# Optimization experiments

Measured on AMD Instinct MI355X. Metric: run time of the kernel, lower is better.

## Reference

```python
import jax, jax.numpy as jnp
import numpy as np

N = 50000        # num nodes
E = 800000       # num edges (avg degree 16)
IN_DIM = 64
OUT_DIM = 64
PE_DIM = 24
HEADS = 2
HID = OUT_DIM * HEADS  # 128


def setup_inputs() -> dict:
    key = jax.random.key(0)
    ks = jax.random.split(key, 16)
    std = 0.1  # trunc_normal_(std=0.1) init in the torch module
    return {
        "x": jax.random.normal(ks[0], (N, IN_DIM), jnp.float32),
        "pe_index": jax.random.randint(ks[1], (2, E), 0, N, jnp.int32),
        "pe_val": jax.random.normal(ks[2], (E, PE_DIM), jnp.float32),
        # edge-weight MLP (blocks): input proj, one residual FFN block, final proj
        "W_in": jax.random.normal(ks[3], (PE_DIM, HID), jnp.float32) * std,
        "b_in": jnp.zeros((HID,), jnp.float32),
        "W1": jax.random.normal(ks[4], (HID, HID), jnp.float32) * std,
        "b1": jnp.zeros((HID,), jnp.float32),
        "W2": jax.random.normal(ks[5], (HID, HID), jnp.float32) * std,
        "b2": jnp.zeros((HID,), jnp.float32),
        "W_fin": jax.random.normal(ks[6], (HID, HID), jnp.float32) * std,
        "b_fin": jnp.zeros((HID,), jnp.float32),
        # node feature -> multi-head projection
        "W_x": jax.random.normal(ks[7], (IN_DIM, HID), jnp.float32) * std,
        "b_x": jnp.zeros((HID,), jnp.float32),
        # per-head output bias
        "head_bias": jnp.zeros((1, HEADS, OUT_DIM), jnp.float32),
        # final out projection
        "W_out": jax.random.normal(ks[8], (HID, OUT_DIM), jnp.float32) * std,
        "b_out": jnp.zeros((OUT_DIM,), jnp.float32),
    }


def _edge_mlp(pe, W_in, b_in, W1, b1, W2, b2, W_fin, b_fin):
    # Linear(pe_dim->hid), then residual block [GELU, Linear, GELU, Linear, +res], then Linear(hid->hid)
    g = lambda t: jax.nn.gelu(t, approximate=False)  # torch nn.GELU default = exact erf
    x0 = pe @ W_in + b_in                     # [E, HID]
    h = g(x0) @ W1 + b1
    h = g(h) @ W2 + b2
    x0 = h + x0                               # ResidualLayer: x + x_res
    return x0 @ W_fin + b_fin                 # [E, HID]


def reference(x, pe_index, pe_val, W_in, b_in, W1, b1, W2, b2, W_fin, b_fin,
              W_x, b_x, head_bias, W_out, b_out):
    tgt = pe_index[0]  # messages aggregate to edge_index[0]
    src = pe_index[1]
    score = _edge_mlp(pe_val, W_in, b_in, W1, b1, W2, b2, W_fin, b_fin)
    score = score.reshape(-1, HEADS, OUT_DIM)                 # [E, H, D]
    xh = (x @ W_x + b_x).reshape(-1, HEADS, OUT_DIM)          # [N, H, D]
    msg = xh[src] * score                                     # gather-multiply
    wV = jax.ops.segment_sum(msg, tgt, num_segments=N)        # scatter-add [N, H, D]
    deg = jax.ops.segment_sum(jnp.ones((msg.shape[0],), jnp.float32), tgt, num_segments=N)
    wV = wV / jnp.maximum(deg, 1.0)[:, None, None]            # average=True -> mean aggregation
    h = (wV + head_bias).reshape(-1, HEADS * OUT_DIM)
    return h @ W_out + b_out                                  # out_proj: [N, OUT_DIM]
```

## Files before the change

### kernel.cpp

```cpp
#include <hip/hip_runtime.h>
#include <hip/hip_bf16.h>
#include <math.h>

#define NN 50000
#define EE 800000
#define HID 128
#define PED 24
#define IND 64
#define OUTD 64
#define EBLK 128
#define AKS 136

typedef short bf16x8 __attribute__((ext_vector_type(8)));
typedef float f32x4 __attribute__((ext_vector_type(4)));

__device__ __forceinline__ float gelu_fast(float x) {
    float x2 = x * x;
    float t = __builtin_fmaf(x2, -0.07135481627f, -1.5957691216f);
    float e = __expf(x * t);
    return x * __builtin_amdgcn_rcpf(1.0f + e);
}
__device__ __forceinline__ unsigned short f2bf(float f) {
    unsigned int u = __float_as_uint(f);
    u = (u + 0x7fffu + ((u >> 16) & 1u)) >> 16;
    return (unsigned short)u;
}
__device__ __forceinline__ unsigned int pkbf2(float a, float b) {
    __hip_bfloat162 h = __float22bfloat162_rn(make_float2(a, b));
    return *reinterpret_cast<unsigned int*>(&h);
}
__device__ __forceinline__ float bflo(unsigned int u) {
    return __uint_as_float(u << 16);
}
__device__ __forceinline__ float bfhi(unsigned int u) {
    return __uint_as_float(u & 0xffff0000u);
}

__global__ __launch_bounds__(256) void pre_kernel(
    const float* __restrict__ x, const float* __restrict__ W_x,
    const float* __restrict__ b_x, unsigned short* __restrict__ xhb,
    const float* __restrict__ W_in, const float* __restrict__ W1,
    const float* __restrict__ W2, const float* __restrict__ Wf,
    unsigned short* __restrict__ WT_in, unsigned short* __restrict__ WT1,
    unsigned short* __restrict__ WT2, unsigned short* __restrict__ WTf,
    float* __restrict__ wV, int* __restrict__ cnt) {
    int bx = blockIdx.x;
    if (bx < 6250) {
        int gid = bx * 256 + threadIdx.x;
        int n = gid >> 5;
        int q = gid & 31;
        *(float4*)&wV[(size_t)n * HID + q * 4] = make_float4(0.f, 0.f, 0.f, 0.f);
        const float* xr = x + (size_t)n * IND;
        float4 acc = *(const float4*)&b_x[q * 4];
#pragma unroll 8
        for (int k = 0; k < IND; k++) {
            float xk = xr[k];
            float4 w = *(const float4*)&W_x[k * HID + q * 4];
            acc.x += xk * w.x; acc.y += xk * w.y;
            acc.z += xk * w.z; acc.w += xk * w.w;
        }
        uint2 p;
        p.x = pkbf2(acc.x, acc.y);
        p.y = pkbf2(acc.z, acc.w);
        ((uint2*)&xhb[(size_t)n * HID])[q] = p;
    } else {
        int idx = (bx - 6250) * 256 + threadIdx.x;
        if (idx < NN) cnt[idx] = 0;
        if (idx < 4096) {
            int j = idx >> 5, k = idx & 31;
            WT_in[idx] = f2bf(k < PED ? W_in[k * HID + j] : 0.f);
        } else if (idx < 4096 + 16384) {
            int i = idx - 4096; int j = i >> 7, k = i & 127;
            WT1[i] = f2bf(W1[k * HID + j]);
        } else if (idx < 4096 + 32768) {
            int i = idx - 4096 - 16384; int j = i >> 7, k = i & 127;
            WT2[i] = f2bf(W2[k * HID + j]);
        } else if (idx < 4096 + 49152) {
            int i = idx - 4096 - 32768; int j = i >> 7, k = i & 127;
            WTf[i] = f2bf(Wf[k * HID + j]);
        }
    }
}

__global__ __launch_bounds__(256) void hist_kernel(const int* __restrict__ pe_idx,
                                                   int* __restrict__ cnt) {
    int e4 = blockIdx.x * 256 + threadIdx.x;
    if (e4 < EE / 4) {
        int4 t = *(const int4*)&pe_idx[e4 * 4];
        atomicAdd(&cnt[t.x], 1);
        atomicAdd(&cnt[t.y], 1);
        atomicAdd(&cnt[t.z], 1);
        atomicAdd(&cnt[t.w], 1);
    }
}

__global__ __launch_bounds__(1024) void scan_kernel(const int* __restrict__ cnt,
                                                    int* __restrict__ woff) {
    __shared__ int s_w[16];
    int tid = threadIdx.x;
    const int chunk = 52;
    int base = tid * chunk;
    int end = base + chunk; if (end > NN) end = NN;
    int s = 0;
    if (base + chunk <= NN) {
#pragma unroll
        for (int i = 0; i < 13; i++) {
            int4 v4 = *(const int4*)&cnt[base + i * 4];
            s += v4.x + v4.y + v4.z + v4.w;
        }
    } else {
        for (int i = base; i < end; i++) s += cnt[i];
    }
    int v = s;
    int lane = tid & 63, wid = tid >> 6;
#pragma unroll
    for (int d = 1; d < 64; d <<= 1) {
        int u = __shfl_up(v, d, 64);
        if (lane >= d) v += u;
    }
    if (lane == 63) s_w[wid] = v;
    __syncthreads();
    if (tid < 16) {
        int wv = s_w[tid];
#pragma unroll
        for (int d = 1; d < 16; d <<= 1) {
            int u = __shfl_up(wv, d, 64);
            if (tid >= d) wv += u;
        }
        s_w[tid] = wv;
    }
    __syncthreads();
    int exc = v - s + (wid ? s_w[wid - 1] : 0);
    int run = exc;
    for (int i = base; i < end; i++) { woff[i] = run; run += cnt[i]; }
}

__global__ __launch_bounds__(256) void scatter_kernel(const int* __restrict__ pe_idx,
                                                      int* __restrict__ woff,
                                                      int* __restrict__ perm) {
    int e4 = blockIdx.x * 256 + threadIdx.x;
    if (e4 < EE / 4) {
        int4 t = *(const int4*)&pe_idx[e4 * 4];
        int e = e4 * 4;
        perm[atomicAdd(&woff[t.x], 1)] = e + 0;
        perm[atomicAdd(&woff[t.y], 1)] = e + 1;
        perm[atomicAdd(&woff[t.z], 1)] = e + 2;
        perm[atomicAdd(&woff[t.w], 1)] = e + 3;
    }
}

__global__ __launch_bounds__(512, 4) void edge_kernel(
    const float* __restrict__ pe_val, const int* __restrict__ pe_idx,
    const int* __restrict__ perm, const unsigned short* __restrict__ xhb,
    const unsigned short* __restrict__ WT_in, const unsigned short* __restrict__ WT1,
    const unsigned short* __restrict__ WT2, const unsigned short* __restrict__ WTf,
    const float* __restrict__ b_in, const float* __restrict__ b1,
    const float* __restrict__ b2, const float* __restrict__ bfin,
    float* __restrict__ wV) {
    __shared__ __align__(16) unsigned short s_act[EBLK][AKS];
    __shared__ __align__(16) unsigned short s_W[HID][AKS];
    __shared__ int s_tgt[EBLK], s_src[EBLK];
    float* s_msg = (float*)&s_W[0][0];

    const int tid = threadIdx.x;
    const int lane = tid & 63;
    const int w = tid >> 6;
    const int cg = w & 3;
    const int eh = w >> 2;
    const int ebase = eh * 64;
    const int l15 = lane & 15;
    const int quad = lane >> 4;
    const long b0 = (long)blockIdx.x * EBLK;

    if (tid < EBLK) {
        int eid = perm[b0 + tid];
        s_tgt[tid] = pe_idx[eid];
        s_src[tid] = pe_idx[EE + eid];
    }
#pragma unroll
    for (int i = 0; i < 4; i++) {
        int idx = tid + i * 512; int r = idx >> 4, seg = idx & 15;
        *(uint4*)&s_W[r][seg * 8] = *(const uint4*)&WT1[r * HID + seg * 8];
    }
#pragma unroll
    for (int i = 0; i < 4; i++) {
        int idx = tid + i * 512; int e = idx >> 4, k2 = idx & 15;
        float2 v = make_float2(0.f, 0.f);
        if (k2 < 12) {
            int eid = perm[b0 + e];
            v = *(const float2*)&pe_val[(size_t)eid * PED + k2 * 2];
        }
        *(unsigned int*)&s_act[e][k2 * 2] = pkbf2(v.x, v.y);
    }
    __syncthreads();

    f32x4 C[2][4];
    uint2 x0pk[2][4];

    {
        float4 ba = *(const float4*)&b_in[(2 * cg + 0) * 16 + quad * 4];
        float4 bb = *(const float4*)&b_in[(2 * cg + 1) * 16 + quad * 4];
        f32x4 ci0 = {ba.x, ba.y, ba.z, ba.w};
        f32x4 ci1 = {bb.x, bb.y, bb.z, bb.w};
        bf16x8 a0 = *(const bf16x8*)&WT_in[((2 * cg + 0) * 16 + l15) * 32 + quad * 8];
        bf16x8 a1 = *(const bf16x8*)&WT_in[((2 * cg + 1) * 16 + l15) * 32 + quad * 8];
        __builtin_amdgcn_s_setprio(1);
#pragma unroll
        for (int u = 0; u < 4; u++) {
            bf16x8 bfr = *(const bf16x8*)&s_act[ebase + u * 16 + l15][quad * 8];
            C[0][u] = __builtin_amdgcn_mfma_f32_16x16x32_bf16(a0, bfr, ci0, 0, 0, 0);
            C[1][u] = __builtin_amdgcn_mfma_f32_16x16x32_bf16(a1, bfr, ci1, 0, 0, 0);
        }
        __builtin_amdgcn_s_setprio(0);
    }
    __syncthreads();
#pragma unroll
    for (int t = 0; t < 2; t++) {
        int ch0 = (2 * cg + t) * 16 + quad * 4;
#pragma unroll
        for (int u = 0; u < 4; u++) {
            int e = ebase + u * 16 + l15;
            f32x4 c = C[t][u];
            x0pk[t][u].x = pkbf2(c[0], c[1]);
            x0pk[t][u].y = pkbf2(c[2], c[3]);
            uint2 p;
            p.x = pkbf2(gelu_fast(c[0]), gelu_fast(c[1]));
            p.y = pkbf2(gelu_fast(c[2]), gelu_fast(c[3]));
            *(uint2*)&s_act[e][ch0] = p;
        }
    }
    __syncthreads();

#define GEMM128(BIAS)                                                          \
    {                                                                          \
        float4 ba_ = *(const float4*)&(BIAS)[(2 * cg + 0) * 16 + quad * 4];    \
        float4 bb_ = *(const float4*)&(BIAS)[(2 * cg + 1) * 16 + quad * 4];    \
        f32x4 ci0 = {ba_.x, ba_.y, ba_.z, ba_.w};                              \
        f32x4 ci1 = {bb_.x, bb_.y, bb_.z, bb_.w};                              \
        _Pragma("unroll") for (int u = 0; u < 4; u++) {                        \
            C[0][u] = ci0; C[1][u] = ci1;                                      \
        }                                                                      \
        __builtin_amdgcn_s_setprio(1);                                         \
        _Pragma("unroll") for (int ks = 0; ks < 4; ks++) {                     \
            bf16x8 a0 = *(const bf16x8*)&s_W[(2 * cg + 0) * 16 + l15]          \
                                            [ks * 32 + quad * 8];              \
            bf16x8 a1 = *(const bf16x8*)&s_W[(2 * cg + 1) * 16 + l15]          \
                                            [ks * 32 + quad * 8];              \
            _Pragma("unroll") for (int u = 0; u < 4; u++) {                    \
                bf16x8 bfr = *(const bf16x8*)&s_act[ebase + u * 16 + l15]      \
                                                   [ks * 32 + quad * 8];       \
                C[0][u] = __builtin_amdgcn_mfma_f32_16x16x32_bf16(a0, bfr,     \
                                                                  C[0][u], 0, 0, 0); \
                C[1][u] = __builtin_amdgcn_mfma_f32_16x16x32_bf16(a1, bfr,     \
                                                                  C[1][u], 0, 0, 0); \
            }                                                                  \
        }                                                                      \
        __builtin_amdgcn_s_setprio(0);                                         \
    }

#define PREFETCH_W(WT, DST)                                                    \
    _Pragma("unroll") for (int i = 0; i < 4; i++) {                            \
        int idx = tid + i * 512;                                               \
        DST[i] = *(const uint4*)&(WT)[(idx >> 4) * HID + (idx & 15) * 8];      \
    }
#define WRITE_W(SRC)                                                           \
    _Pragma("unroll") for (int i = 0; i < 4; i++) {                            \
        int idx = tid + i * 512; int r = idx >> 4, seg = idx & 15;             \
        *(uint4*)&s_W[r][seg * 8] = SRC[i];                                    \
    }

    uint4 wpre[4];
    PREFETCH_W(WT2, wpre);
    GEMM128(b1);
    __syncthreads();
#pragma unroll
    for (int t = 0; t < 2; t++) {
        int ch0 = (2 * cg + t) * 16 + quad * 4;
#pragma unroll
        for (int u = 0; u < 4; u++) {
            int e = ebase + u * 16 + l15;
            f32x4 c = C[t][u];
            uint2 p;
            p.x = pkbf2(gelu_fast(c[0]), gelu_fast(c[1]));
            p.y = pkbf2(gelu_fast(c[2]), gelu_fast(c[3]));
            *(uint2*)&s_act[e][ch0] = p;
        }
    }
    WRITE_W(wpre);
    __syncthreads();

    PREFETCH_W(WTf, wpre);
    GEMM128(b2);
    __syncthreads();
#pragma unroll
    for (int t = 0; t < 2; t++) {
        int ch0 = (2 * cg + t) * 16 + quad * 4;
#pragma unroll
        for (int u = 0; u < 4; u++) {
            int e = ebase + u * 16 + l15;
            f32x4 c = C[t][u];
            uint2 p;
            p.x = pkbf2(c[0] + bflo(x0pk[t][u].x), c[1] + bfhi(x0pk[t][u].x));
            p.y = pkbf2(c[2] + bflo(x0pk[t][u].y), c[3] + bfhi(x0pk[t][u].y));
            *(uint2*)&s_act[e][ch0] = p;
        }
    }
    WRITE_W(wpre);
    __syncthreads();

    GEMM128(bfin);
    uint2 xva[4];
#pragma unroll
    for (int i = 0; i < 4; i++) {
        int idx = tid + i * 512; int e = idx >> 5, c4 = idx & 31;
        xva[i] = ((const uint2*)&xhb[(size_t)s_src[e] * HID])[c4];
    }
    __syncthreads();
#pragma unroll
    for (int t = 0; t < 2; t++) {
        int ch0 = (2 * cg + t) * 16 + quad * 4;
#pragma unroll
        for (int u = 0; u < 4; u++) {
            int e = ebase + u * 16 + l15;
            f32x4 c = C[t][u];
            uint2 p;
            p.x = pkbf2(c[0], c[1]);
            p.y = pkbf2(c[2], c[3]);
            *(uint2*)&s_act[e][ch0] = p;
        }
    }
    __syncthreads();

#pragma unroll
    for (int i = 0; i < 4; i++) {
        int idx = tid + i * 512;
        int e = idx >> 5, c4 = idx & 31;
        uint2 xv = xva[i];
        uint2 sv = *(const uint2*)&s_act[e][c4 * 4];
        float4 m;
        m.x = bflo(xv.x) * bflo(sv.x);
        m.y = bfhi(xv.x) * bfhi(sv.x);
        m.z = bflo(xv.y) * bflo(sv.y);
        m.w = bfhi(xv.y) * bfhi(sv.y);
        *(float4*)&s_msg[e * HID + c4 * 4] = m;
    }
    uint2 xvb[4];
#pragma unroll
    for (int i = 0; i < 4; i++) {
        int idx = tid + (4 + i) * 512; int e = idx >> 5, c4 = idx & 31;
        xvb[i] = ((const uint2*)&xhb[(size_t)s_src[e] * HID])[c4];
    }
    __syncthreads();

    if (tid < 256) {
        const int h = tid >> 7;
        const int c = tid & 127;
        const int e0 = h * 32;
        float acc = 0.f;
        int prev = s_tgt[e0];
        bool firstseg = true;
        for (int e = e0; e < e0 + 32; e++) {
            int tg = s_tgt[e];
            if (tg != prev) {
                if (firstseg) atomicAdd(&wV[(size_t)prev * HID + c], acc);
                else          wV[(size_t)prev * HID + c] = acc;
                firstseg = false;
                acc = 0.f;
                prev = tg;
            }
            acc += s_msg[e * HID + c];
        }
        atomicAdd(&wV[(size_t)prev * HID + c], acc);
    }
    __syncthreads();

#pragma unroll
    for (int i = 0; i < 4; i++) {
        int idx = tid + (4 + i) * 512;
        int e = idx >> 5, c4 = idx & 31;
        uint2 xv = xvb[i];
        uint2 sv = *(const uint2*)&s_act[e][c4 * 4];
        float4 m;
        m.x = bflo(xv.x) * bflo(sv.x);
        m.y = bfhi(xv.x) * bfhi(sv.x);
        m.z = bflo(xv.y) * bflo(sv.y);
        m.w = bfhi(xv.y) * bfhi(sv.y);
        *(float4*)&s_msg[(e - 64) * HID + c4 * 4] = m;
    }
    __syncthreads();

    if (tid < 256) {
        const int h = tid >> 7;
        const int c = tid & 127;
        const int e0 = 64 + h * 32;
        float acc = 0.f;
        int prev = s_tgt[e0];
        bool firstseg = true;
        for (int e = e0; e < e0 + 32; e++) {
            int tg = s_tgt[e];
            if (tg != prev) {
                if (firstseg) atomicAdd(&wV[(size_t)prev * HID + c], acc);
                else          wV[(size_t)prev * HID + c] = acc;
                firstseg = false;
                acc = 0.f;
                prev = tg;
            }
            acc += s_msg[(e - 64) * HID + c];
        }
        atomicAdd(&wV[(size_t)prev * HID + c], acc);
    }
#undef GEMM128
#undef PREFETCH_W
#undef WRITE_W
}

__global__ __launch_bounds__(256) void out_kernel(
    const float* __restrict__ wV, const int* __restrict__ cnt,
    const float* __restrict__ head_bias, const float* __restrict__ W_out,
    const float* __restrict__ b_out, float* __restrict__ out) {
    int gid = blockIdx.x * 256 + threadIdx.x;
    int n = gid >> 4;
    int q = gid & 15;
    if (n >= NN) return;
    float inv = 1.0f / fmaxf((float)cnt[n], 1.0f);
    const float* wr = wV + (size_t)n * HID;
    float4 acc = *(const float4*)&b_out[q * 4];
#pragma unroll 4
    for (int k = 0; k < HID; k++) {
        float hv = wr[k] * inv + head_bias[k];
        float4 wv4 = *(const float4*)&W_out[k * OUTD + q * 4];
        acc.x += hv * wv4.x; acc.y += hv * wv4.y;
        acc.z += hv * wv4.z; acc.w += hv * wv4.w;
    }
    *(float4*)&out[(size_t)n * OUTD + q * 4] = acc;
}

extern "C" void kernel_launch(void* const* d_in, const int* in_sizes, int n_in,
                              void* d_out, int out_size, void* d_ws, size_t ws_size,
                              hipStream_t stream) {
    const float* x      = (const float*)d_in[0];
    const int*   pe_idx = (const int*)d_in[1];
    const float* pe_val = (const float*)d_in[2];
    const float* W_in   = (const float*)d_in[3];
    const float* b_in   = (const float*)d_in[4];
    const float* W1     = (const float*)d_in[5];
    const float* b1     = (const float*)d_in[6];
    const float* W2     = (const float*)d_in[7];
    const float* b2     = (const float*)d_in[8];
    const float* Wf     = (const float*)d_in[9];
    const float* bfin   = (const float*)d_in[10];
    const float* W_x    = (const float*)d_in[11];
    const float* b_x    = (const float*)d_in[12];
    const float* hb     = (const float*)d_in[13];
    const float* W_out  = (const float*)d_in[14];
    const float* b_out  = (const float*)d_in[15];
    float* out = (float*)d_out;

    float* wV   = (float*)d_ws;
    int*   cnt  = (int*)(wV + (size_t)NN * HID);
    int*   woff = cnt + NN;
    int*   perm = woff + NN;
    unsigned short* WT_in = (unsigned short*)(perm + EE);
    unsigned short* WT1   = WT_in + 128 * 32;
    unsigned short* WT2   = WT1 + 128 * 128;
    unsigned short* WTf   = WT2 + 128 * 128;
    unsigned short* xhb   = WTf + 128 * 128;

    pre_kernel<<<6250 + 208, 256, 0, stream>>>(x, W_x, b_x, xhb,
                                               W_in, W1, W2, Wf,
                                               WT_in, WT1, WT2, WTf, wV, cnt);
    hist_kernel<<<(EE / 4 + 255) / 256, 256, 0, stream>>>(pe_idx, cnt);
    scan_kernel<<<1, 1024, 0, stream>>>(cnt, woff);
    scatter_kernel<<<(EE / 4 + 255) / 256, 256, 0, stream>>>(pe_idx, woff, perm);

    edge_kernel<<<EE / EBLK, 512, 0, stream>>>(pe_val, pe_idx, perm, xhb,
                                               WT_in, WT1, WT2, WTf,
                                               b_in, b1, b2, bfin, wV);

    out_kernel<<<(NN * 16 + 255) / 256, 256, 0, stream>>>(wV, cnt, hb, W_out,
                                                          b_out, out);
}
```

Before: 693.5 us.

## Register-tile node GEMMs with shared weights and drop edge weight prefetch

The node projection in pre_kernel and the output projection in out_kernel now stage the weight matrix in shared memory. Each thread computes four nodes, so every weight load is reused across several rows instead of being re-read from global memory per node. In the edge kernel, the register prefetch of the next layer's weights is replaced by a direct global-to-shared copy after the epilogue. That lowers register pressure but exposes the load latency between the GEMM stages.

```diff
diff --git a/kernel.cpp b/kernel.cpp
--- a/kernel.cpp
+++ b/kernel.cpp
@@ -10,6 +10,8 @@
 #define OUTD 64
 #define EBLK 128
 #define AKS 136
+#define XNB 32
+#define ONB 64
 
 typedef short bf16x8 __attribute__((ext_vector_type(8)));
 typedef float f32x4 __attribute__((ext_vector_type(4)));
@@ -36,6 +38,7 @@
     return __uint_as_float(u & 0xffff0000u);
 }
 
+#define XHB ((NN + XNB - 1) / XNB)
 __global__ __launch_bounds__(256) void pre_kernel(
     const float* __restrict__ x, const float* __restrict__ W_x,
     const float* __restrict__ b_x, unsigned short* __restrict__ xhb,
@@ -45,26 +48,64 @@
     unsigned short* __restrict__ WT2, unsigned short* __restrict__ WTf,
     float* __restrict__ wV, int* __restrict__ cnt) {
     int bx = blockIdx.x;
-    if (bx < 6250) {
-        int gid = bx * 256 + threadIdx.x;
-        int n = gid >> 5;
-        int q = gid & 31;
-        *(float4*)&wV[(size_t)n * HID + q * 4] = make_float4(0.f, 0.f, 0.f, 0.f);
-        const float* xr = x + (size_t)n * IND;
-        float4 acc = *(const float4*)&b_x[q * 4];
-#pragma unroll 8
-        for (int k = 0; k < IND; k++) {
-            float xk = xr[k];
-            float4 w = *(const float4*)&W_x[k * HID + q * 4];
-            acc.x += xk * w.x; acc.y += xk * w.y;
-            acc.z += xk * w.z; acc.w += xk * w.w;
-        }
-        uint2 p;
-        p.x = pkbf2(acc.x, acc.y);
-        p.y = pkbf2(acc.z, acc.w);
-        ((uint2*)&xhb[(size_t)n * HID])[q] = p;
+    int tid = threadIdx.x;
+    if (bx < XHB) {
+        __shared__ float s_Wx[IND * HID];
+#pragma unroll
+        for (int i = 0; i < 8; i++) {
+            int idx = tid + i * 256;
+            *(float4*)&s_Wx[idx * 4] = *(const float4*)&W_x[idx * 4];
+        }
+#pragma unroll
+        for (int i = 0; i < 4; i++) {
+            int idx = tid + i * 256;
+            int n = bx * XNB + (idx >> 5);
+            if (n < NN)
+                *(float4*)&wV[(size_t)n * HID + (idx & 31) * 4] =
+                    make_float4(0.f, 0.f, 0.f, 0.f);
+        }
+        __syncthreads();
+        const int g = tid >> 5;
+        const int q = tid & 31;
+        const int nb = bx * XNB + g * 4;
+        float4 bb = *(const float4*)&b_x[q * 4];
+        f32x4 acc[4];
+        int nc[4];
+#pragma unroll
+        for (int j = 0; j < 4; j++) {
+            acc[j] = (f32x4){bb.x, bb.y, bb.z, bb.w};
+            int n = nb + j;
+            nc[j] = n < NN ? n : NN - 1;
+        }
+#pragma unroll
+        for (int k4 = 0; k4 < 16; k4++) {
+            float4 xv[4];
+#pragma unroll
+            for (int j = 0; j < 4; j++)
+                xv[j] = *(const float4*)&x[(size_t)nc[j] * IND + k4 * 4];
+#pragma unroll
+            for (int kk = 0; kk < 4; kk++) {
+                float4 w4 = *(const float4*)&s_Wx[(k4 * 4 + kk) * HID + q * 4];
+#pragma unroll
+                for (int j = 0; j < 4; j++) {
+                    float xs = ((const float*)&xv[j])[kk];
+                    acc[j][0] += xs * w4.x; acc[j][1] += xs * w4.y;
+                    acc[j][2] += xs * w4.z; acc[j][3] += xs * w4.w;
+                }
+            }
+        }
+#pragma unroll
+        for (int j = 0; j < 4; j++) {
+            int n = nb + j;
+            if (n < NN) {
+                uint2 p;
+                p.x = pkbf2(acc[j][0], acc[j][1]);
+                p.y = pkbf2(acc[j][2], acc[j][3]);
+                *(uint2*)&xhb[(size_t)n * HID + q * 4] = p;
+            }
+        }
     } else {
-        int idx = (bx - 6250) * 256 + threadIdx.x;
+        int idx = (bx - XHB) * 256 + tid;
         if (idx < NN) cnt[idx] = 0;
         if (idx < 4096) {
             int j = idx >> 5, k = idx & 31;
@@ -258,19 +299,12 @@
         __builtin_amdgcn_s_setprio(0);                                         \
     }
 
-#define PREFETCH_W(WT, DST)                                                    \
-    _Pragma("unroll") for (int i = 0; i < 4; i++) {                            \
-        int idx = tid + i * 512;                                               \
-        DST[i] = *(const uint4*)&(WT)[(idx >> 4) * HID + (idx & 15) * 8];      \
-    }
-#define WRITE_W(SRC)                                                           \
+#define STAGE_W(WT)                                                            \
     _Pragma("unroll") for (int i = 0; i < 4; i++) {                            \
         int idx = tid + i * 512; int r = idx >> 4, seg = idx & 15;             \
-        *(uint4*)&s_W[r][seg * 8] = SRC[i];                                    \
-    }
-
-    uint4 wpre[4];
-    PREFETCH_W(WT2, wpre);
+        *(uint4*)&s_W[r][seg * 8] = *(const uint4*)&(WT)[r * HID + seg * 8];   \
+    }
+
     GEMM128(b1);
     __syncthreads();
 #pragma unroll
@@ -286,10 +320,9 @@
             *(uint2*)&s_act[e][ch0] = p;
         }
     }
-    WRITE_W(wpre);
-    __syncthreads();
-
-    PREFETCH_W(WTf, wpre);
+    STAGE_W(WT2);
+    __syncthreads();
+
     GEMM128(b2);
     __syncthreads();
 #pragma unroll
@@ -305,7 +338,7 @@
             *(uint2*)&s_act[e][ch0] = p;
         }
     }
-    WRITE_W(wpre);
+    STAGE_W(WTf);
     __syncthreads();
 
     GEMM128(bfin);
@@ -410,29 +443,65 @@
         atomicAdd(&wV[(size_t)prev * HID + c], acc);
     }
 #undef GEMM128
-#undef PREFETCH_W
-#undef WRITE_W
+#undef STAGE_W
 }
 
 __global__ __launch_bounds__(256) void out_kernel(
     const float* __restrict__ wV, const int* __restrict__ cnt,
     const float* __restrict__ head_bias, const float* __restrict__ W_out,
     const float* __restrict__ b_out, float* __restrict__ out) {
-    int gid = blockIdx.x * 256 + threadIdx.x;
-    int n = gid >> 4;
-    int q = gid & 15;
-    if (n >= NN) return;
-    float inv = 1.0f / fmaxf((float)cnt[n], 1.0f);
-    const float* wr = wV + (size_t)n * HID;
-    float4 acc = *(const float4*)&b_out[q * 4];
-#pragma unroll 4
-    for (int k = 0; k < HID; k++) {
-        float hv = wr[k] * inv + head_bias[k];
-        float4 wv4 = *(const float4*)&W_out[k * OUTD + q * 4];
-        acc.x += hv * wv4.x; acc.y += hv * wv4.y;
-        acc.z += hv * wv4.z; acc.w += hv * wv4.w;
-    }
-    *(float4*)&out[(size_t)n * OUTD + q * 4] = acc;
+    __shared__ float s_Wo[HID * OUTD];
+    __shared__ float s_hb[HID];
+    int tid = threadIdx.x;
+#pragma unroll
+    for (int i = 0; i < 8; i++) {
+        int idx = tid + i * 256;
+        *(float4*)&s_Wo[idx * 4] = *(const float4*)&W_out[idx * 4];
+    }
+    if (tid < 32) *(float4*)&s_hb[tid * 4] = *(const float4*)&head_bias[tid * 4];
+    __syncthreads();
+
+    const int g = tid >> 4;
+    const int q = tid & 15;
+    const int nb = blockIdx.x * ONB + g * 4;
+    float4 bb = *(const float4*)&b_out[q * 4];
+    f32x4 acc[4];
+    float inv[4];
+    int nc[4];
+#pragma unroll
+    for (int j = 0; j < 4; j++) {
+        acc[j] = (f32x4){bb.x, bb.y, bb.z, bb.w};
+        int n = nb + j;
+        nc[j] = n < NN ? n : NN - 1;
+        inv[j] = 1.0f / fmaxf((float)cnt[nc[j]], 1.0f);
+    }
+#pragma unroll
+    for (int k4 = 0; k4 < 32; k4++) {
+        float4 wrv[4];
+#pragma unroll
+        for (int j = 0; j < 4; j++)
+            wrv[j] = *(const float4*)&wV[(size_t)nc[j] * HID + k4 * 4];
+#pragma unroll
+        for (int kk = 0; kk < 4; kk++) {
+            int k = k4 * 4 + kk;
+            float4 w4 = *(const float4*)&s_Wo[k * OUTD + q * 4];
+            float hbk = s_hb[k];
+#pragma unroll
+            for (int j = 0; j < 4; j++) {
+                float hv = __builtin_fmaf(((const float*)&wrv[j])[kk], inv[j], hbk);
+                acc[j][0] += hv * w4.x; acc[j][1] += hv * w4.y;
+                acc[j][2] += hv * w4.z; acc[j][3] += hv * w4.w;
+            }
+        }
+    }
+#pragma unroll
+    for (int j = 0; j < 4; j++) {
+        int n = nb + j;
+        if (n < NN) {
+            float4 o = {acc[j][0], acc[j][1], acc[j][2], acc[j][3]};
+            *(float4*)&out[(size_t)n * OUTD + q * 4] = o;
+        }
+    }
 }
 
 extern "C" void kernel_launch(void* const* d_in, const int* in_sizes, int n_in,
@@ -466,9 +535,9 @@
     unsigned short* WTf   = WT2 + 128 * 128;
     unsigned short* xhb   = WTf + 128 * 128;
 
-    pre_kernel<<<6250 + 208, 256, 0, stream>>>(x, W_x, b_x, xhb,
-                                               W_in, W1, W2, Wf,
-                                               WT_in, WT1, WT2, WTf, wV, cnt);
+    pre_kernel<<<XHB + 208, 256, 0, stream>>>(x, W_x, b_x, xhb,
+                                              W_in, W1, W2, Wf,
+                                              WT_in, WT1, WT2, WTf, wV, cnt);
     hist_kernel<<<(EE / 4 + 255) / 256, 256, 0, stream>>>(pe_idx, cnt);
     scan_kernel<<<1, 1024, 0, stream>>>(cnt, woff);
     scatter_kernel<<<(EE / 4 + 255) / 256, 256, 0, stream>>>(pe_idx, woff, perm);
@@ -477,6 +546,6 @@
                                                WT_in, WT1, WT2, WTf,
                                                b_in, b1, b2, bfin, wV);
 
-    out_kernel<<<(NN * 16 + 255) / 256, 256, 0, stream>>>(wV, cnt, hb, W_out,
-                                                          b_out, out);
-}
+    out_kernel<<<(NN + ONB - 1) / ONB, 256, 0, stream>>>(wV, cnt, hb, W_out,
+                                                         b_out, out);
+}
```

After: 1.148 ms. 1.65x slower.

## Fuse message multiply with per-wave segmented reduction and drop weight register prefetch

Applied to the files above, without the earlier changes.

The message multiply and the segmented scatter-add are merged. Each wave now owns 16 consecutive sorted edges and accumulates the products of gathered xh and score straight into registers, with no fp32 message buffer in shared memory, fewer block barriers, and all 512 threads doing the reduction instead of 256. The pe input gets its own shared buffer, so one barrier after the first GEMM can go. Weight staging now copies global to shared directly instead of prefetching into registers during the previous GEMM. That gives up load/compute overlap in exchange for fewer live registers, and wave-level segments may add atomics at segment boundaries.

```diff
diff --git a/kernel.cpp b/kernel.cpp
--- a/kernel.cpp
+++ b/kernel.cpp
@@ -159,8 +159,8 @@
     float* __restrict__ wV) {
     __shared__ __align__(16) unsigned short s_act[EBLK][AKS];
     __shared__ __align__(16) unsigned short s_W[HID][AKS];
+    __shared__ __align__(16) unsigned short s_pe[EBLK][32];
     __shared__ int s_tgt[EBLK], s_src[EBLK];
-    float* s_msg = (float*)&s_W[0][0];
 
     const int tid = threadIdx.x;
     const int lane = tid & 63;
@@ -190,7 +190,7 @@
             int eid = perm[b0 + e];
             v = *(const float2*)&pe_val[(size_t)eid * PED + k2 * 2];
         }
-        *(unsigned int*)&s_act[e][k2 * 2] = pkbf2(v.x, v.y);
+        *(unsigned int*)&s_pe[e][k2 * 2] = pkbf2(v.x, v.y);
     }
     __syncthreads();
 
@@ -207,13 +207,12 @@
         __builtin_amdgcn_s_setprio(1);
 #pragma unroll
         for (int u = 0; u < 4; u++) {
-            bf16x8 bfr = *(const bf16x8*)&s_act[ebase + u * 16 + l15][quad * 8];
+            bf16x8 bfr = *(const bf16x8*)&s_pe[ebase + u * 16 + l15][quad * 8];
             C[0][u] = __builtin_amdgcn_mfma_f32_16x16x32_bf16(a0, bfr, ci0, 0, 0, 0);
             C[1][u] = __builtin_amdgcn_mfma_f32_16x16x32_bf16(a1, bfr, ci1, 0, 0, 0);
         }
         __builtin_amdgcn_s_setprio(0);
     }
-    __syncthreads();
 #pragma unroll
     for (int t = 0; t < 2; t++) {
         int ch0 = (2 * cg + t) * 16 + quad * 4;
@@ -258,19 +257,12 @@
         __builtin_amdgcn_s_setprio(0);                                         \
     }
 
-#define PREFETCH_W(WT, DST)                                                    \
-    _Pragma("unroll") for (int i = 0; i < 4; i++) {                            \
-        int idx = tid + i * 512;                                               \
-        DST[i] = *(const uint4*)&(WT)[(idx >> 4) * HID + (idx & 15) * 8];      \
-    }
-#define WRITE_W(SRC)                                                           \
+#define STAGE_W(WT)                                                            \
     _Pragma("unroll") for (int i = 0; i < 4; i++) {                            \
         int idx = tid + i * 512; int r = idx >> 4, seg = idx & 15;             \
-        *(uint4*)&s_W[r][seg * 8] = SRC[i];                                    \
-    }
-
-    uint4 wpre[4];
-    PREFETCH_W(WT2, wpre);
+        *(uint4*)&s_W[r][seg * 8] = *(const uint4*)&(WT)[r * HID + seg * 8];   \
+    }
+
     GEMM128(b1);
     __syncthreads();
 #pragma unroll
@@ -286,10 +278,9 @@
             *(uint2*)&s_act[e][ch0] = p;
         }
     }
-    WRITE_W(wpre);
-    __syncthreads();
-
-    PREFETCH_W(WTf, wpre);
+    STAGE_W(WT2);
+    __syncthreads();
+
     GEMM128(b2);
     __syncthreads();
 #pragma unroll
@@ -305,15 +296,15 @@
             *(uint2*)&s_act[e][ch0] = p;
         }
     }
-    WRITE_W(wpre);
+    STAGE_W(WTf);
     __syncthreads();
 
     GEMM128(bfin);
-    uint2 xva[4];
-#pragma unroll
-    for (int i = 0; i < 4; i++) {
-        int idx = tid + i * 512; int e = idx >> 5, c4 = idx & 31;
-        xva[i] = ((const uint2*)&xhb[(size_t)s_src[e] * HID])[c4];
+    const int e0 = w * 16;
+    unsigned int xv[16];
+#pragma unroll
+    for (int j = 0; j < 16; j++) {
+        xv[j] = *(const unsigned int*)&xhb[(size_t)s_src[e0 + j] * HID + lane * 2];
     }
     __syncthreads();
 #pragma unroll
@@ -331,87 +322,31 @@
     }
     __syncthreads();
 
-#pragma unroll
-    for (int i = 0; i < 4; i++) {
-        int idx = tid + i * 512;
-        int e = idx >> 5, c4 = idx & 31;
-        uint2 xv = xva[i];
-        uint2 sv = *(const uint2*)&s_act[e][c4 * 4];
-        float4 m;
-        m.x = bflo(xv.x) * bflo(sv.x);
-        m.y = bfhi(xv.x) * bfhi(sv.x);
-        m.z = bflo(xv.y) * bflo(sv.y);
-        m.w = bfhi(xv.y) * bfhi(sv.y);
-        *(float4*)&s_msg[e * HID + c4 * 4] = m;
-    }
-    uint2 xvb[4];
-#pragma unroll
-    for (int i = 0; i < 4; i++) {
-        int idx = tid + (4 + i) * 512; int e = idx >> 5, c4 = idx & 31;
-        xvb[i] = ((const uint2*)&xhb[(size_t)s_src[e] * HID])[c4];
-    }
-    __syncthreads();
-
-    if (tid < 256) {
-        const int h = tid >> 7;
-        const int c = tid & 127;
-        const int e0 = h * 32;
-        float acc = 0.f;
+    {
+        float a0 = 0.f, a1 = 0.f;
         int prev = s_tgt[e0];
         bool firstseg = true;
-        for (int e = e0; e < e0 + 32; e++) {
-            int tg = s_tgt[e];
+#pragma unroll
+        for (int j = 0; j < 16; j++) {
+            int tg = s_tgt[e0 + j];
             if (tg != prev) {
-                if (firstseg) atomicAdd(&wV[(size_t)prev * HID + c], acc);
-                else          wV[(size_t)prev * HID + c] = acc;
+                float* wp = &wV[(size_t)prev * HID + lane * 2];
+                if (firstseg) { atomicAdd(wp, a0); atomicAdd(wp + 1, a1); }
+                else          { *(float2*)wp = make_float2(a0, a1); }
                 firstseg = false;
-                acc = 0.f;
+                a0 = a1 = 0.f;
                 prev = tg;
             }
-            acc += s_msg[e * HID + c];
-        }
-        atomicAdd(&wV[(size_t)prev * HID + c], acc);
-    }
-    __syncthreads();
-
-#pragma unroll
-    for (int i = 0; i < 4; i++) {
-        int idx = tid + (4 + i) * 512;
-        int e = idx >> 5, c4 = idx & 31;
-        uint2 xv = xvb[i];
-        uint2 sv = *(const uint2*)&s_act[e][c4 * 4];
-        float4 m;
-        m.x = bflo(xv.x) * bflo(sv.x);
-        m.y = bfhi(xv.x) * bfhi(sv.x);
-        m.z = bflo(xv.y) * bflo(sv.y);
-        m.w = bfhi(xv.y) * bfhi(sv.y);
-        *(float4*)&s_msg[(e - 64) * HID + c4 * 4] = m;
-    }
-    __syncthreads();
-
-    if (tid < 256) {
-        const int h = tid >> 7;
-        const int c = tid & 127;
-        const int e0 = 64 + h * 32;
-        float acc = 0.f;
-        int prev = s_tgt[e0];
-        bool firstseg = true;
-        for (int e = e0; e < e0 + 32; e++) {
-            int tg = s_tgt[e];
-            if (tg != prev) {
-                if (firstseg) atomicAdd(&wV[(size_t)prev * HID + c], acc);
-                else          wV[(size_t)prev * HID + c] = acc;
-                firstseg = false;
-                acc = 0.f;
-                prev = tg;
-            }
-            acc += s_msg[(e - 64) * HID + c];
-        }
-        atomicAdd(&wV[(size_t)prev * HID + c], acc);
+            unsigned int sv = *(const unsigned int*)&s_act[e0 + j][lane * 2];
+            unsigned int xu = xv[j];
+            a0 += bflo(xu) * bflo(sv);
+            a1 += bfhi(xu) * bfhi(sv);
+        }
+        float* wp = &wV[(size_t)prev * HID + lane * 2];
+        atomicAdd(wp, a0); atomicAdd(wp + 1, a1);
     }
 #undef GEMM128
-#undef PREFETCH_W
-#undef WRITE_W
+#undef STAGE_W
 }
 
 __global__ __launch_bounds__(256) void out_kernel(
```

After: 592.9 us. 14.5% less time.
